# Kernel optimization log

Measured on AMD Instinct MI355X. Metric: run time of the kernel, lower is better.

Reference implementation:

```python
import jax, jax.numpy as jnp
import numpy as np

B, NV, L = 64, 8, 1024
P = 16            # patch_len == stride (non-overlapping)
D, H, DFF = 768, 12, 3072
K = D // H        # head dim 64
T = L // P        # 64 patches per sequence
N = B * NV        # 512 flattened sequences


def _ln(x, g, b, eps=1e-5):
    m = x.mean(-1, keepdims=True)
    v = x.var(-1, keepdims=True)
    return (x - m) / jnp.sqrt(v + eps) * g + b


def _pos_emb():
    pos = jnp.arange(T, dtype=jnp.float32)[:, None]
    div = jnp.exp(jnp.arange(0, D, 2, dtype=jnp.float32) * (-np.log(10000.0) / D))
    pe = jnp.zeros((T, D), jnp.float32)
    pe = pe.at[:, 0::2].set(jnp.sin(pos * div))
    pe = pe.at[:, 1::2].set(jnp.cos(pos * div))
    return pe


def setup_inputs() -> dict:
    key = jax.random.key(0)
    ks = jax.random.split(key, 24)
    rn = lambda k, s: jax.random.normal(k, s, jnp.float32) * 0.02
    return dict(
        x=jax.random.normal(ks[0], (B, NV, L), jnp.float32),
        W_patch=rn(ks[1], (P, D)), b_patch=jnp.zeros((D,), jnp.float32),
        ln1_g=jnp.ones((D,), jnp.float32), ln1_b=jnp.zeros((D,), jnp.float32),
        ln2_g=jnp.ones((D,), jnp.float32), ln2_b=jnp.zeros((D,), jnp.float32),
        mu_r=jax.random.uniform(ks[2], (D,), jnp.float32),
        mu_w=jax.random.uniform(ks[3], (D,), jnp.float32),
        mu_k=jax.random.uniform(ks[4], (D,), jnp.float32),
        mu_v=jax.random.uniform(ks[5], (D,), jnp.float32),
        mu_a=jax.random.uniform(ks[6], (D,), jnp.float32),
        mu_g=jax.random.uniform(ks[7], (D,), jnp.float32),
        mu_c=jax.random.uniform(ks[8], (D,), jnp.float32),
        Wr=rn(ks[9], (D, D)), Wk=rn(ks[10], (D, D)), Wv=rn(ks[11], (D, D)),
        Wg=rn(ks[12], (D, D)), Ww=rn(ks[13], (D, D)), w0=rn(ks[14], (D,)),
        Wa=rn(ks[15], (D, D)), a0=jnp.zeros((D,), jnp.float32),
        Wo=rn(ks[16], (D, D)),
        gn_g=jnp.ones((D,), jnp.float32), gn_b=jnp.zeros((D,), jnp.float32),
        Wc1=rn(ks[17], (D, DFF)), Wc2=rn(ks[18], (DFF, D)),
        W_proj=rn(ks[19], (D, P)), b_proj=jnp.zeros((P,), jnp.float32),
    )


def reference(x, W_patch, b_patch, ln1_g, ln1_b, ln2_g, ln2_b,
              mu_r, mu_w, mu_k, mu_v, mu_a, mu_g, mu_c,
              Wr, Wk, Wv, Wg, Ww, w0, Wa, a0, Wo, gn_g, gn_b,
              Wc1, Wc2, W_proj, b_proj):
    # --- patch embedding (stride == patch_len -> plain reshape) ---
    patches = x.reshape(B, NV, T, P).reshape(N, T, P)
    h = patches @ W_patch + b_patch + _pos_emb()        # [N, T, D]

    # --- RWKV7 time mixing ---
    xx = _ln(h, ln1_g, ln1_b)
    sh = jnp.pad(xx[:, :-1], ((0, 0), (1, 0), (0, 0)))  # token shift
    lerp = lambda mu: xx + (sh - xx) * mu
    r = (lerp(mu_r) @ Wr).reshape(N, T, H, K)
    k = (lerp(mu_k) @ Wk).reshape(N, T, H, K)
    v = (lerp(mu_v) @ Wv).reshape(N, T, H, K)
    w = jnp.exp(-jnp.exp(lerp(mu_w) @ Ww + w0)).reshape(N, T, H, K)  # decay in (0,1)
    a = jax.nn.sigmoid(lerp(mu_a) @ Wa + a0).reshape(N, T, H, K)     # in-context lr
    g = jax.nn.sigmoid(lerp(mu_g) @ Wg)                              # output gate [N,T,D]
    kk = k / (jnp.linalg.norm(k, axis=-1, keepdims=True) + 1e-6)     # removal key

    seq = tuple(jnp.transpose(t, (1, 0, 2, 3)) for t in (r, w, k, v, kk, a))

    def step(S, inp):
        # S: [N, H, V, K] value-by-key state (generalized delta rule)
        r_t, w_t, k_t, v_t, kk_t, a_t = inp
        S = S * w_t[:, :, None, :]
        sa = jnp.einsum('nhvk,nhk->nhv', S, kk_t)
        S = S - jnp.einsum('nhv,nhk->nhvk', sa, kk_t * a_t) \
              + jnp.einsum('nhv,nhk->nhvk', v_t, k_t)
        y = jnp.einsum('nhvk,nhk->nhv', S, r_t)
        return S, y

    S0 = jnp.zeros((N, H, K, K), x.dtype)
    _, ys = jax.lax.scan(step, S0, seq)
    y = jnp.transpose(ys, (1, 0, 2, 3))                 # [N, T, H, K]

    # per-head group norm (RWKV7 uses eps = 64e-5)
    m = y.mean(-1, keepdims=True)
    var = y.var(-1, keepdims=True)
    y = (y - m) / jnp.sqrt(var + 64e-5)
    y = y.reshape(N, T, D) * gn_g + gn_b
    h = h + (y * g) @ Wo

    # --- channel mixing (squared-ReLU FFN) ---
    xc = _ln(h, ln2_g, ln2_b)
    shc = jnp.pad(xc[:, :-1], ((0, 0), (1, 0), (0, 0)))
    xk = xc + (shc - xc) * mu_c
    h = h + jnp.square(jax.nn.relu(xk @ Wc1)) @ Wc2

    # --- projection back to patch space ---
    return h @ W_proj + b_proj                          # [N, T, P]
```

## Files before the change

kernel.cpp:

```cpp
#include <hip/hip_runtime.h>
#include <hip/hip_bf16.h>
#include <math.h>

typedef unsigned short u16;
typedef unsigned int u32;
typedef _Float16 f16x8 __attribute__((ext_vector_type(8)));
typedef float f32x4 __attribute__((ext_vector_type(4)));

#define DEV static __device__ __forceinline__

constexpr int D = 768;
constexpr int HH = 12;
constexpr int KD = 64;
constexpr int T = 64;
constexpr int NSEQ = 512;
constexpr int MROWS = NSEQ * T;
constexpr int DFF = 3072;
constexpr int PP = 16;

DEV u16 f2h(float f){ union{_Float16 h; u16 u;} c; c.h = (_Float16)f; return c.u; }
DEV float h2f(u16 u){ union{u16 u; _Float16 h;} c; c.u = u; return (float)c.h; }
DEV void gld_lds16(const u16* g, u16* l){
  __builtin_amdgcn_global_load_lds((const __attribute__((address_space(1))) void*)g,
                                   (__attribute__((address_space(3))) void*)l, 16, 0, 0);
}
DEV int lsw(int row, int kgrp){ return row * 32 + ((((row >> 2) ^ row) & 3) ^ kgrp) * 8; }

struct TpArgs { const float* src[7]; u16* dst[7]; };
__global__ __launch_bounds__(256) void k_transpose7(TpArgs a){
  __shared__ float tile[32][33];
  int z = blockIdx.z;
  const float* W = a.src[z];
  u16* WT = a.dst[z];
  int c0 = blockIdx.x * 32, r0 = blockIdx.y * 32;
  int tx = threadIdx.x, ty = threadIdx.y;
  #pragma unroll
  for (int i = 0; i < 32; i += 8)
    tile[ty + i][tx] = W[(size_t)(r0 + ty + i) * D + (c0 + tx)];
  __syncthreads();
  #pragma unroll
  for (int i = 0; i < 32; i += 8)
    WT[(size_t)(c0 + ty + i) * D + (r0 + tx)] = f2h(tile[tx][ty + i]);
}

__global__ __launch_bounds__(256) void k_transpose(const float* __restrict__ W, u16* __restrict__ WT,
                                                   int R, int C){
  __shared__ float tile[32][33];
  int c0 = blockIdx.x * 32, r0 = blockIdx.y * 32;
  int tx = threadIdx.x, ty = threadIdx.y;
  #pragma unroll
  for (int i = 0; i < 32; i += 8)
    tile[ty + i][tx] = W[(size_t)(r0 + ty + i) * C + (c0 + tx)];
  __syncthreads();
  #pragma unroll
  for (int i = 0; i < 32; i += 8)
    WT[(size_t)(c0 + ty + i) * R + (r0 + tx)] = f2h(tile[tx][ty + i]);
}

__global__ void k_pe(float* __restrict__ pe){
  int idx = blockIdx.x * 256 + threadIdx.x;
  if (idx >= T * D) return;
  int t = idx / D, d = idx % D;
  float dv = __expf((float)(d & ~1) * (-9.210340371976184f / (float)D));
  float ang = (float)t * dv;
  pe[idx] = (d & 1) ? cosf(ang) : sinf(ang);
}

struct MuArgs { const float* mu[6]; };
__global__ __launch_bounds__(256) void k_mu16(MuArgs a, u16* __restrict__ mu16){
  int z = blockIdx.x;
  #pragma unroll
  for (int j = 0; j < 3; j++){
    int d = threadIdx.x + j * 256;
    mu16[z * D + d] = f2h(a.mu[z][d]);
  }
}

__global__ __launch_bounds__(256) void k_patch_ln(const float* __restrict__ x, const float* __restrict__ Wp,
                                                  const float* __restrict__ bp, const float* __restrict__ pe,
                                                  const float* __restrict__ g, const float* __restrict__ b,
                                                  float* __restrict__ h, u16* __restrict__ xx16){
  int lane = threadIdx.x & 63;
  int row = blockIdx.x * 4 + (threadIdx.x >> 6);
  int t = row & (T - 1);
  const float* xr = x + (size_t)row * PP;
  float xs[PP];
  #pragma unroll
  for (int p = 0; p < PP; p++) xs[p] = xr[p];
  float v[12], s = 0.f, sq = 0.f;
  #pragma unroll
  for (int j = 0; j < 12; j++){
    int d = lane + j * 64;
    float acc = bp[d] + pe[t * D + d];
    #pragma unroll
    for (int p = 0; p < PP; p++) acc = fmaf(xs[p], Wp[p * D + d], acc);
    v[j] = acc; s += acc; sq = fmaf(acc, acc, sq);
  }
  #pragma unroll
  for (int o = 32; o; o >>= 1){ s += __shfl_xor(s, o); sq += __shfl_xor(sq, o); }
  float mean = s * (1.f / 768.f);
  float rstd = rsqrtf(sq * (1.f / 768.f) - mean * mean + 1e-5f);
  float* hrow = h + (size_t)row * D;
  u16* xrow = xx16 + (size_t)row * D;
  #pragma unroll
  for (int j = 0; j < 12; j++){
    int d = lane + j * 64;
    hrow[d] = v[j];
    xrow[d] = f2h((v[j] - mean) * rstd * g[d] + b[d]);
  }
}

__global__ __launch_bounds__(256) void k_ln2(const float* __restrict__ X, const float* __restrict__ g,
                                             const float* __restrict__ b, const float* __restrict__ mu,
                                             u16* __restrict__ out){
  int lane = threadIdx.x & 63;
  int row = blockIdx.x * 4 + (threadIdx.x >> 6);
  int t = row & (T - 1);
  const float* xr = X + (size_t)row * D;
  float v[12], s = 0.f, sq = 0.f;
  #pragma unroll
  for (int j = 0; j < 12; j++){ v[j] = xr[lane + j * 64]; s += v[j]; sq += v[j] * v[j]; }
  #pragma unroll
  for (int o = 32; o; o >>= 1){ s += __shfl_xor(s, o); sq += __shfl_xor(sq, o); }
  float mean = s * (1.f / 768.f);
  float rstd = rsqrtf(sq * (1.f / 768.f) - mean * mean + 1e-5f);
  float p[12], meanp = 0.f, rstdp = 0.f;
  if (t){
    const float* xp = xr - D;
    float sp = 0.f, sqp = 0.f;
    #pragma unroll
    for (int j = 0; j < 12; j++){ p[j] = xp[lane + j * 64]; sp += p[j]; sqp += p[j] * p[j]; }
    #pragma unroll
    for (int o = 32; o; o >>= 1){ sp += __shfl_xor(sp, o); sqp += __shfl_xor(sqp, o); }
    meanp = sp * (1.f / 768.f);
    rstdp = rsqrtf(sqp * (1.f / 768.f) - meanp * meanp + 1e-5f);
  }
  u16* orow = out + (size_t)row * D;
  #pragma unroll
  for (int j = 0; j < 12; j++){
    int d = lane + j * 64;
    float cm = (v[j] - mean) * rstd * g[d] + b[d];
    float cp = t ? (p[j] - meanp) * rstdp * g[d] + b[d] : 0.f;
    orow[d] = f2h(cm + (cp - cm) * mu[d]);
  }
}

template<int ACT>
__global__ __launch_bounds__(256) void k_g16(const u16* __restrict__ A, const u16* __restrict__ BT,
                                             u16* __restrict__ outH, float* __restrict__ outF,
                                             int Kd, int Nc){
  __shared__ __align__(16) u16 As[128 * 32];
  __shared__ __align__(16) u16 Bs[128 * 32];
  int tid = threadIdx.x;
  int m0 = blockIdx.x * 128, n0 = blockIdx.y * 128;
  int wv = tid >> 6, lane = tid & 63;
  int wr = (wv >> 1) * 64, wc = (wv & 1) * 64;
  int lr = lane & 15, kgrp = lane >> 4;
  int r0 = wv * 16 + (lane >> 2);
  int cbg = ((((r0 >> 2) ^ r0) & 3) ^ (lane & 3)) * 8;
  const u16* sA0 = A + (size_t)(m0 + r0) * Kd + cbg;
  const u16* sA1 = A + (size_t)(m0 + r0 + 64) * Kd + cbg;
  const u16* sB0 = BT + (size_t)(n0 + r0) * Kd + cbg;
  const u16* sB1 = BT + (size_t)(n0 + r0 + 64) * Kd + cbg;
  int cb = (lane & 3) * 8;
  u16* dA0 = As + r0 * 32 + cb;
  u16* dA1 = As + (r0 + 64) * 32 + cb;
  u16* dB0 = Bs + r0 * 32 + cb;
  u16* dB1 = Bs + (r0 + 64) * 32 + cb;
  f32x4 acc[4][4] = {};

  for (int k0 = 0; k0 < Kd; k0 += 32){
    __syncthreads();
    gld_lds16(sA0 + k0, dA0);
    gld_lds16(sA1 + k0, dA1);
    gld_lds16(sB0 + k0, dB0);
    gld_lds16(sB1 + k0, dB1);
    __syncthreads();
    f16x8 af[4], bf[4];
    #pragma unroll
    for (int mi = 0; mi < 4; mi++) af[mi] = *(const f16x8*)&As[lsw(wr + mi * 16 + lr, kgrp)];
    #pragma unroll
    for (int ni = 0; ni < 4; ni++) bf[ni] = *(const f16x8*)&Bs[lsw(wc + ni * 16 + lr, kgrp)];
    #pragma unroll
    for (int mi = 0; mi < 4; mi++){
      #pragma unroll
      for (int ni = 0; ni < 4; ni++){
        acc[mi][ni] = __builtin_amdgcn_mfma_f32_16x16x32_f16(af[mi], bf[ni], acc[mi][ni], 0, 0, 0);
      }
    }
  }

  int rowb = m0 + wr + (lane >> 4) * 4;
  int colb = n0 + wc + lr;
  #pragma unroll
  for (int mi = 0; mi < 4; mi++){
    #pragma unroll
    for (int ni = 0; ni < 4; ni++){
      int gcol = colb + ni * 16;
      #pragma unroll
      for (int i = 0; i < 4; i++){
        int grow = rowb + mi * 16 + i;
        float xv = acc[mi][ni][i];
        size_t o = (size_t)grow * Nc + gcol;
        if (ACT == 3){ float rl = fmaxf(xv, 0.f); outH[o] = f2h(rl * rl); }
        else outF[o] += xv;
      }
    }
  }
}

struct MixArgs {
  const u16* b[6]; const float* bias[6]; const u16* mu16;
  u16* outh[6]; int act[6];
};
__global__ __launch_bounds__(256) void k_mix_lerp(const u16* __restrict__ X16, MixArgs args, int Kd, int Nc){
  __shared__ __align__(16) u16 As[128 * 32];
  __shared__ __align__(16) u16 Bs[128 * 32];
  int tid = threadIdx.x, z = blockIdx.z;
  const u16* BT = args.b[z];
  const u16* mu16 = args.mu16 + z * D;
  int m0 = blockIdx.x * 128, n0 = blockIdx.y * 128;
  int wv = tid >> 6, lane = tid & 63;
  int wr = (wv >> 1) * 64, wc = (wv & 1) * 64;
  int lr = lane & 15, kgrp = lane >> 4;
  int r0 = wv * 16 + (lane >> 2);
  int cbg = ((((r0 >> 2) ^ r0) & 3) ^ (lane & 3)) * 8;
  const u16* sB0 = BT + (size_t)(n0 + r0) * Kd + cbg;
  const u16* sB1 = BT + (size_t)(n0 + r0 + 64) * Kd + cbg;
  int cb = (lane & 3) * 8;
  u16* dB0 = Bs + r0 * 32 + cb;
  u16* dB1 = Bs + (r0 + 64) * 32 + cb;
  f32x4 acc[4][4] = {};

  for (int k0 = 0; k0 < Kd; k0 += 32){
    __syncthreads();
    gld_lds16(sB0 + k0, dB0);
    gld_lds16(sB1 + k0, dB1);
    #pragma unroll
    for (int pass = 0; pass < 2; pass++){
      int c = pass * 256 + tid;
      int rr = c >> 2, cgrp = c & 3, c8 = cgrp * 8;
      int row = m0 + rr;
      bool tnz = (row & (T - 1)) != 0;
      const u16* src = X16 + (size_t)row * Kd + k0 + c8;
      f16x8 cur = *(const f16x8*)src;
      f16x8 m8 = *(const f16x8*)(mu16 + k0 + c8);
      f16x8 res;
      if (tnz){
        f16x8 prv = *(const f16x8*)(src - Kd);
        res = cur + (prv - cur) * m8;
      } else {
        res = cur - cur * m8;
      }
      *(f16x8*)&As[lsw(rr, cgrp)] = res;
    }
    __syncthreads();
    f16x8 af[4], bf[4];
    #pragma unroll
    for (int mi = 0; mi < 4; mi++) af[mi] = *(const f16x8*)&As[lsw(wr + mi * 16 + lr, kgrp)];
    #pragma unroll
    for (int ni = 0; ni < 4; ni++) bf[ni] = *(const f16x8*)&Bs[lsw(wc + ni * 16 + lr, kgrp)];
    #pragma unroll
    for (int mi = 0; mi < 4; mi++){
      #pragma unroll
      for (int ni = 0; ni < 4; ni++){
        acc[mi][ni] = __builtin_amdgcn_mfma_f32_16x16x32_f16(af[mi], bf[ni], acc[mi][ni], 0, 0, 0);
      }
    }
  }

  int act = args.act[z];
  const float* bias = args.bias[z];
  u16* outh = args.outh[z];
  int rowb = m0 + wr + (lane >> 4) * 4;
  int colb = n0 + wc + lr;
  #pragma unroll
  for (int mi = 0; mi < 4; mi++){
    #pragma unroll
    for (int ni = 0; ni < 4; ni++){
      int gcol = colb + ni * 16;
      float bv = bias ? bias[gcol] : 0.f;
      #pragma unroll
      for (int i = 0; i < 4; i++){
        int grow = rowb + mi * 16 + i;
        float xv = acc[mi][ni][i] + bv;
        size_t o = (size_t)grow * Nc + gcol;
        if (act == 2) xv = 1.f / (1.f + __expf(-xv));
        outh[o] = f2h(xv);
      }
    }
  }
}

constexpr int TS = 8;
__global__ __launch_bounds__(256) void k_rwkv(const u16* __restrict__ rb16, const u16* __restrict__ wp16,
                                              const u16* __restrict__ kb16, const u16* __restrict__ vb,
                                              const u16* __restrict__ ab, const u16* __restrict__ gbuf,
                                              const float* __restrict__ gng, const float* __restrict__ gnb,
                                              u16* __restrict__ yg){
  __shared__ __align__(16) float ls_w[TS][64], ls_k[TS][64], ls_r[TS][64];
  __shared__ float ls_v[TS][64];
  __shared__ float ls_kk[TS][64], ls_ka[TS][64];
  __shared__ float sa_red[2][4][64];
  __shared__ float y_red[2][4][64];
  int nh = blockIdx.x;
  int n = nh / HH, hh = nh - n * HH;
  int tid = threadIdx.x;
  int wv = __builtin_amdgcn_readfirstlane(tid >> 6);
  int lane = tid & 63;
  float S[16];
  #pragma unroll
  for (int i = 0; i < 16; i++) S[i] = 0.f;
  int dcol = hh * KD + lane;
  float gscale = gng[dcol], gshift = gnb[dcol];
  size_t hbase = (size_t)n * T * D + hh * KD;
  int jbase = wv * 16;
  int strow = tid >> 5;
  int stcol = (tid & 31) * 2;
  for (int tt = 0; tt < T; tt += TS){
    __syncthreads();
    size_t gofs = hbase + (size_t)(tt + strow) * D + stcol;
    u32 w2 = *(const u32*)(wp16 + gofs);
    u32 k2 = *(const u32*)(kb16 + gofs);
    u32 r2 = *(const u32*)(rb16 + gofs);
    u32 v2 = *(const u32*)(vb + gofs);
    u32 a2 = *(const u32*)(ab + gofs);
    float k0 = h2f((u16)(k2 & 0xffffu));
    float k1 = h2f((u16)(k2 >> 16));
    float ss = fmaf(k0, k0, k1 * k1);
    #pragma unroll
    for (int o = 16; o; o >>= 1) ss += __shfl_xor(ss, o);
    float inv = 1.f / (sqrtf(ss) + 1e-6f);
    float kk0 = k0 * inv, kk1 = k1 * inv;
    ls_w[strow][stcol]     = __expf(-__expf(h2f((u16)(w2 & 0xffffu))));
    ls_w[strow][stcol + 1] = __expf(-__expf(h2f((u16)(w2 >> 16))));
    ls_k[strow][stcol]     = k0;
    ls_k[strow][stcol + 1] = k1;
    ls_r[strow][stcol]     = h2f((u16)(r2 & 0xffffu));
    ls_r[strow][stcol + 1] = h2f((u16)(r2 >> 16));
    ls_v[strow][stcol]     = h2f((u16)(v2 & 0xffffu));
    ls_v[strow][stcol + 1] = h2f((u16)(v2 >> 16));
    ls_kk[strow][stcol]     = kk0;
    ls_kk[strow][stcol + 1] = kk1;
    ls_ka[strow][stcol]     = kk0 * h2f((u16)(a2 & 0xffffu));
    ls_ka[strow][stcol + 1] = kk1 * h2f((u16)(a2 >> 16));
    __syncthreads();
    for (int s = 0; s < TS; s++){
      int sg = tt + s;
      int pb = sg & 1;
      f32x4 W4[4], KK4[4];
      #pragma unroll
      for (int q = 0; q < 4; q++){
        W4[q]  = *(const f32x4*)&ls_w[s][jbase + q * 4];
        KK4[q] = *(const f32x4*)&ls_kk[s][jbase + q * 4];
      }
      float sap = 0.f;
      #pragma unroll
      for (int q = 0; q < 4; q++){
        #pragma unroll
        for (int i = 0; i < 4; i++){
          S[q * 4 + i] *= W4[q][i];
          sap += S[q * 4 + i] * KK4[q][i];
        }
      }
      sa_red[pb][wv][lane] = sap;
      __syncthreads();
      if (wv == 0 && sg > 0){
        int pp = pb ^ 1;
        float y = y_red[pp][0][lane] + y_red[pp][1][lane] + y_red[pp][2][lane] + y_red[pp][3][lane];
        float s1 = y, s2 = y * y;
        #pragma unroll
        for (int o = 32; o; o >>= 1){ s1 += __shfl_xor(s1, o); s2 += __shfl_xor(s2, o); }
        float mean = s1 * (1.f / 64.f);
        float var = s2 * (1.f / 64.f) - mean * mean;
        float yn = (y - mean) * rsqrtf(var + 64e-5f);
        size_t pidx = hbase + (size_t)(sg - 1) * D + lane;
        float gv = h2f(gbuf[pidx]);
        yg[pidx] = f2h((yn * gscale + gshift) * gv);
      }
      float sa = sa_red[pb][0][lane] + sa_red[pb][1][lane] + sa_red[pb][2][lane] + sa_red[pb][3][lane];
      float nsa = -sa;
      float vl = ls_v[s][lane];
      f32x4 K4[4], KA4[4], R4[4];
      #pragma unroll
      for (int q = 0; q < 4; q++){
        K4[q]  = *(const f32x4*)&ls_k[s][jbase + q * 4];
        KA4[q] = *(const f32x4*)&ls_ka[s][jbase + q * 4];
        R4[q]  = *(const f32x4*)&ls_r[s][jbase + q * 4];
      }
      float yp = 0.f;
      #pragma unroll
      for (int q = 0; q < 4; q++){
        #pragma unroll
        for (int i = 0; i < 4; i++){
          S[q * 4 + i] = fmaf(vl, K4[q][i], S[q * 4 + i]);
          S[q * 4 + i] = fmaf(nsa, KA4[q][i], S[q * 4 + i]);
          yp += S[q * 4 + i] * R4[q][i];
        }
      }
      y_red[pb][wv][lane] = yp;
    }
  }
  __syncthreads();
  if (wv == 0){
    int pp = (T - 1) & 1;
    float y = y_red[pp][0][lane] + y_red[pp][1][lane] + y_red[pp][2][lane] + y_red[pp][3][lane];
    float s1 = y, s2 = y * y;
    #pragma unroll
    for (int o = 32; o; o >>= 1){ s1 += __shfl_xor(s1, o); s2 += __shfl_xor(s2, o); }
    float mean = s1 * (1.f / 64.f);
    float var = s2 * (1.f / 64.f) - mean * mean;
    float yn = (y - mean) * rsqrtf(var + 64e-5f);
    size_t pidx = hbase + (size_t)(T - 1) * D + lane;
    float gv = h2f(gbuf[pidx]);
    yg[pidx] = f2h((yn * gscale + gshift) * gv);
  }
}

__global__ __launch_bounds__(256) void k_proj(const float* __restrict__ Hb, const float* __restrict__ Wp,
                                              const float* __restrict__ bp, float* __restrict__ out){
  int lane = threadIdx.x & 63;
  int row = blockIdx.x * 4 + (threadIdx.x >> 6);
  int p = lane & 15, q = lane >> 4;
  const float* hr = Hb + (size_t)row * D;
  float acc = 0.f;
  #pragma unroll 8
  for (int i = 0; i < 192; i++){
    int d = q * 192 + i;
    acc = fmaf(hr[d], Wp[d * PP + p], acc);
  }
  acc += __shfl_xor(acc, 16);
  acc += __shfl_xor(acc, 32);
  if (q == 0) out[(size_t)row * PP + p] = acc + bp[p];
}

extern "C" void kernel_launch(void* const* d_in, const int* in_sizes, int n_in,
                              void* d_out, int out_size, void* d_ws, size_t ws_size,
                              hipStream_t stream){
  (void)in_sizes; (void)n_in; (void)out_size;
  const float* x       = (const float*)d_in[0];
  const float* W_patch = (const float*)d_in[1];
  const float* b_patch = (const float*)d_in[2];
  const float* ln1_g   = (const float*)d_in[3];
  const float* ln1_b   = (const float*)d_in[4];
  const float* ln2_g   = (const float*)d_in[5];
  const float* ln2_b   = (const float*)d_in[6];
  const float* mu_r    = (const float*)d_in[7];
  const float* mu_w    = (const float*)d_in[8];
  const float* mu_k    = (const float*)d_in[9];
  const float* mu_v    = (const float*)d_in[10];
  const float* mu_a    = (const float*)d_in[11];
  const float* mu_g    = (const float*)d_in[12];
  const float* mu_c    = (const float*)d_in[13];
  const float* Wr      = (const float*)d_in[14];
  const float* Wk      = (const float*)d_in[15];
  const float* Wv      = (const float*)d_in[16];
  const float* Wg      = (const float*)d_in[17];
  const float* Ww      = (const float*)d_in[18];
  const float* w0      = (const float*)d_in[19];
  const float* Wa      = (const float*)d_in[20];
  const float* a0      = (const float*)d_in[21];
  const float* Wo      = (const float*)d_in[22];
  const float* gn_g    = (const float*)d_in[23];
  const float* gn_b    = (const float*)d_in[24];
  const float* Wc1     = (const float*)d_in[25];
  const float* Wc2     = (const float*)d_in[26];
  const float* W_proj  = (const float*)d_in[27];
  const float* b_proj  = (const float*)d_in[28];
  float* out = (float*)d_out;

  char* ws = (char*)d_ws;
  size_t off = 0;
  auto alloc = [&](size_t bytes) -> char* {
    char* p = ws + off;
    off = (off + bytes + 255) & ~(size_t)255;
    return p;
  };

  const size_t WB = (size_t)D * D * 2;
  u16* WrT  = (u16*)alloc(WB);
  u16* WwT  = (u16*)alloc(WB);
  u16* WkT  = (u16*)alloc(WB);
  u16* WvT  = (u16*)alloc(WB);
  u16* WaT  = (u16*)alloc(WB);
  u16* WgT  = (u16*)alloc(WB);
  u16* WoT  = (u16*)alloc(WB);
  u16* Wc1T = (u16*)alloc((size_t)D * DFF * 2);
  u16* Wc2T = (u16*)alloc((size_t)DFF * D * 2);
  float* pe = (float*)alloc((size_t)T * D * 4);
  u16* mu16 = (u16*)alloc((size_t)6 * D * 2);
  size_t wend = off;

  int nch = 1;
  size_t Mc = MROWS;
  while (nch < 128){
    size_t need = wend + Mc * 13824 + 64 * 256;
    if (need <= ws_size) break;
    nch *= 2;
    Mc >>= 1;
  }
  float* hbuf = (float*)alloc(Mc * 768 * 4);
  u16* xx     = (u16*)alloc(Mc * 768 * 2);
  u16* wp     = (u16*)alloc(Mc * 768 * 2);
  u16* rb     = (u16*)alloc(Mc * 768 * 2);
  u16* kb     = (u16*)alloc(Mc * 768 * 2);
  u16* vb     = (u16*)alloc(Mc * 768 * 2);
  u16* ab     = (u16*)alloc(Mc * 768 * 2);
  u16* gb     = (u16*)alloc(Mc * 768 * 2);
  u16* ygb = ab;
  u16* mid = xx;
  u16* xkb = gb;

  dim3 tb(32, 8);
  TpArgs ta;
  ta.src[0] = Wr; ta.dst[0] = WrT;
  ta.src[1] = Ww; ta.dst[1] = WwT;
  ta.src[2] = Wk; ta.dst[2] = WkT;
  ta.src[3] = Wv; ta.dst[3] = WvT;
  ta.src[4] = Wa; ta.dst[4] = WaT;
  ta.src[5] = Wg; ta.dst[5] = WgT;
  ta.src[6] = Wo; ta.dst[6] = WoT;
  k_transpose7<<<dim3(24, 24, 7), tb, 0, stream>>>(ta);
  k_transpose<<<dim3(96, 24), tb, 0, stream>>>(Wc1, Wc1T, D, DFF);
  k_transpose<<<dim3(24, 96), tb, 0, stream>>>(Wc2, Wc2T, DFF, D);
  k_pe<<<dim3(192), dim3(256), 0, stream>>>(pe);
  MuArgs ma;
  ma.mu[0] = mu_r; ma.mu[1] = mu_w; ma.mu[2] = mu_k;
  ma.mu[3] = mu_v; ma.mu[4] = mu_a; ma.mu[5] = mu_g;
  k_mu16<<<dim3(6), dim3(256), 0, stream>>>(ma, mu16);

  MixArgs margs;
  const u16* wts[6] = {WrT, WwT, WkT, WvT, WaT, WgT};
  const float* bss[6] = {nullptr, w0, nullptr, nullptr, a0, nullptr};
  u16* oh[6] = {rb, wp, kb, vb, ab, gb};
  int acts[6] = {0, 1, 0, 0, 2, 2};
  margs.mu16 = mu16;
  for (int z = 0; z < 6; z++){
    margs.b[z] = wts[z];
    margs.bias[z] = bss[z];
    margs.outh[z] = oh[z];
    margs.act[z] = acts[z];
  }

  for (int c = 0; c < nch; ++c){
    const float* xc = x + (size_t)c * Mc * PP;
    float* outc = out + (size_t)c * Mc * PP;
    int mcb = (int)(Mc / 128);

    k_patch_ln<<<dim3((int)(Mc / 4)), dim3(256), 0, stream>>>(xc, W_patch, b_patch, pe, ln1_g, ln1_b, hbuf, xx);

    k_mix_lerp<<<dim3(mcb, 6, 6), 256, 0, stream>>>(xx, margs, D, D);

    k_rwkv<<<dim3((int)(Mc / T) * HH), dim3(256), 0, stream>>>(rb, wp, kb, vb, ab, gb, gn_g, gn_b, ygb);

    k_g16<4><<<dim3(mcb, 6), 256, 0, stream>>>(ygb, WoT, nullptr, hbuf, D, D);

    k_ln2<<<dim3((int)(Mc / 4)), dim3(256), 0, stream>>>(hbuf, ln2_g, ln2_b, mu_c, xkb);
    k_g16<3><<<dim3(mcb, DFF / 128), 256, 0, stream>>>(xkb, Wc1T, mid, nullptr, D, DFF);
    k_g16<4><<<dim3(mcb, 6), 256, 0, stream>>>(mid, Wc2T, nullptr, hbuf, DFF, D);

    k_proj<<<dim3((int)(Mc / 4)), dim3(256), 0, stream>>>(hbuf, W_proj, b_proj, outc);
  }
}
```

Measured before the change: 1.737 ms.

## Double-buffer LDS tiles in GEMM and mix-lerp kernels to overlap loads with MFMA

Both the plain fp16 GEMM and the token-shift lerp GEMM now keep two LDS buffers for the A and B tiles. The next K-slice is prefetched (via global_load_lds, or register loads followed by the lerp and an LDS store) while MFMAs run on the current slice, and each iteration needs one barrier instead of two. This is meant to hide global-load latency behind compute. In exchange the kernels use twice the LDS, which may lower occupancy, and the lerp kernel holds more registers live across the loop.

```diff
diff --git a/kernel.cpp b/kernel.cpp
--- a/kernel.cpp
+++ b/kernel.cpp
@@ -149,8 +149,8 @@
 __global__ __launch_bounds__(256) void k_g16(const u16* __restrict__ A, const u16* __restrict__ BT,
                                              u16* __restrict__ outH, float* __restrict__ outF,
                                              int Kd, int Nc){
-  __shared__ __align__(16) u16 As[128 * 32];
-  __shared__ __align__(16) u16 Bs[128 * 32];
+  __shared__ __align__(16) u16 As[2][128 * 32];
+  __shared__ __align__(16) u16 Bs[2][128 * 32];
   int tid = threadIdx.x;
   int m0 = blockIdx.x * 128, n0 = blockIdx.y * 128;
   int wv = tid >> 6, lane = tid & 63;
@@ -163,24 +163,29 @@
   const u16* sB0 = BT + (size_t)(n0 + r0) * Kd + cbg;
   const u16* sB1 = BT + (size_t)(n0 + r0 + 64) * Kd + cbg;
   int cb = (lane & 3) * 8;
-  u16* dA0 = As + r0 * 32 + cb;
-  u16* dA1 = As + (r0 + 64) * 32 + cb;
-  u16* dB0 = Bs + r0 * 32 + cb;
-  u16* dB1 = Bs + (r0 + 64) * 32 + cb;
+  int o0 = r0 * 32 + cb, o1 = (r0 + 64) * 32 + cb;
   f32x4 acc[4][4] = {};
-
-  for (int k0 = 0; k0 < Kd; k0 += 32){
-    __syncthreads();
-    gld_lds16(sA0 + k0, dA0);
-    gld_lds16(sA1 + k0, dA1);
-    gld_lds16(sB0 + k0, dB0);
-    gld_lds16(sB1 + k0, dB1);
-    __syncthreads();
+  int NT = Kd >> 5;
+
+  gld_lds16(sA0, &As[0][o0]);
+  gld_lds16(sA1, &As[0][o1]);
+  gld_lds16(sB0, &Bs[0][o0]);
+  gld_lds16(sB1, &Bs[0][o1]);
+  __syncthreads();
+  int cur = 0;
+  for (int kt = 0; kt < NT; kt++){
+    if (kt + 1 < NT){
+      int k0 = (kt + 1) << 5;
+      gld_lds16(sA0 + k0, &As[cur ^ 1][o0]);
+      gld_lds16(sA1 + k0, &As[cur ^ 1][o1]);
+      gld_lds16(sB0 + k0, &Bs[cur ^ 1][o0]);
+      gld_lds16(sB1 + k0, &Bs[cur ^ 1][o1]);
+    }
     f16x8 af[4], bf[4];
     #pragma unroll
-    for (int mi = 0; mi < 4; mi++) af[mi] = *(const f16x8*)&As[lsw(wr + mi * 16 + lr, kgrp)];
-    #pragma unroll
-    for (int ni = 0; ni < 4; ni++) bf[ni] = *(const f16x8*)&Bs[lsw(wc + ni * 16 + lr, kgrp)];
+    for (int mi = 0; mi < 4; mi++) af[mi] = *(const f16x8*)&As[cur][lsw(wr + mi * 16 + lr, kgrp)];
+    #pragma unroll
+    for (int ni = 0; ni < 4; ni++) bf[ni] = *(const f16x8*)&Bs[cur][lsw(wc + ni * 16 + lr, kgrp)];
     #pragma unroll
     for (int mi = 0; mi < 4; mi++){
       #pragma unroll
@@ -188,6 +193,8 @@
         acc[mi][ni] = __builtin_amdgcn_mfma_f32_16x16x32_f16(af[mi], bf[ni], acc[mi][ni], 0, 0, 0);
       }
     }
+    __syncthreads();
+    cur ^= 1;
   }
 
   int rowb = m0 + wr + (lane >> 4) * 4;
@@ -214,8 +221,8 @@
   u16* outh[6]; int act[6];
 };
 __global__ __launch_bounds__(256) void k_mix_lerp(const u16* __restrict__ X16, MixArgs args, int Kd, int Nc){
-  __shared__ __align__(16) u16 As[128 * 32];
-  __shared__ __align__(16) u16 Bs[128 * 32];
+  __shared__ __align__(16) u16 As[2][128 * 32];
+  __shared__ __align__(16) u16 Bs[2][128 * 32];
   int tid = threadIdx.x, z = blockIdx.z;
   const u16* BT = args.b[z];
   const u16* mu16 = args.mu16 + z * D;
@@ -228,38 +235,54 @@
   const u16* sB0 = BT + (size_t)(n0 + r0) * Kd + cbg;
   const u16* sB1 = BT + (size_t)(n0 + r0 + 64) * Kd + cbg;
   int cb = (lane & 3) * 8;
-  u16* dB0 = Bs + r0 * 32 + cb;
-  u16* dB1 = Bs + (r0 + 64) * 32 + cb;
+  int o0 = r0 * 32 + cb, o1 = (r0 + 64) * 32 + cb;
+  int rr0 = tid >> 2, cg0 = tid & 3;
+  int rr1 = (256 + tid) >> 2, cg1 = (256 + tid) & 3;
+  bool tz0 = ((m0 + rr0) & (T - 1)) != 0;
+  bool tz1 = ((m0 + rr1) & (T - 1)) != 0;
+  const u16* srcA0 = X16 + (size_t)(m0 + rr0) * Kd + cg0 * 8;
+  const u16* srcA1 = X16 + (size_t)(m0 + rr1) * Kd + cg1 * 8;
+  int wsl0 = lsw(rr0, cg0), wsl1 = lsw(rr1, cg1);
   f32x4 acc[4][4] = {};
-
-  for (int k0 = 0; k0 < Kd; k0 += 32){
-    __syncthreads();
-    gld_lds16(sB0 + k0, dB0);
-    gld_lds16(sB1 + k0, dB1);
-    #pragma unroll
-    for (int pass = 0; pass < 2; pass++){
-      int c = pass * 256 + tid;
-      int rr = c >> 2, cgrp = c & 3, c8 = cgrp * 8;
-      int row = m0 + rr;
-      bool tnz = (row & (T - 1)) != 0;
-      const u16* src = X16 + (size_t)row * Kd + k0 + c8;
-      f16x8 cur = *(const f16x8*)src;
-      f16x8 m8 = *(const f16x8*)(mu16 + k0 + c8);
-      f16x8 res;
-      if (tnz){
-        f16x8 prv = *(const f16x8*)(src - Kd);
-        res = cur + (prv - cur) * m8;
-      } else {
-        res = cur - cur * m8;
-      }
-      *(f16x8*)&As[lsw(rr, cgrp)] = res;
-    }
-    __syncthreads();
+  int NT = Kd >> 5;
+
+  gld_lds16(sB0, &Bs[0][o0]);
+  gld_lds16(sB1, &Bs[0][o1]);
+  {
+    f16x8 c0 = *(const f16x8*)srcA0;
+    f16x8 m0v = *(const f16x8*)(mu16 + cg0 * 8);
+    f16x8 p0 = {};
+    if (tz0) p0 = *(const f16x8*)(srcA0 - Kd);
+    *(f16x8*)&As[0][wsl0] = c0 + (p0 - c0) * m0v;
+    f16x8 c1 = *(const f16x8*)srcA1;
+    f16x8 m1v = *(const f16x8*)(mu16 + cg1 * 8);
+    f16x8 p1 = {};
+    if (tz1) p1 = *(const f16x8*)(srcA1 - Kd);
+    *(f16x8*)&As[0][wsl1] = c1 + (p1 - c1) * m1v;
+  }
+  __syncthreads();
+  int cur = 0;
+  for (int kt = 0; kt < NT; kt++){
+    bool hn = (kt + 1 < NT);
+    f16x8 nc0, np0, nm0, nc1, np1, nm1;
+    if (hn){
+      int k0 = (kt + 1) << 5;
+      gld_lds16(sB0 + k0, &Bs[cur ^ 1][o0]);
+      gld_lds16(sB1 + k0, &Bs[cur ^ 1][o1]);
+      nc0 = *(const f16x8*)(srcA0 + k0);
+      nm0 = *(const f16x8*)(mu16 + k0 + cg0 * 8);
+      np0 = f16x8{};
+      if (tz0) np0 = *(const f16x8*)(srcA0 + k0 - Kd);
+      nc1 = *(const f16x8*)(srcA1 + k0);
+      nm1 = *(const f16x8*)(mu16 + k0 + cg1 * 8);
+      np1 = f16x8{};
+      if (tz1) np1 = *(const f16x8*)(srcA1 + k0 - Kd);
+    }
     f16x8 af[4], bf[4];
     #pragma unroll
-    for (int mi = 0; mi < 4; mi++) af[mi] = *(const f16x8*)&As[lsw(wr + mi * 16 + lr, kgrp)];
-    #pragma unroll
-    for (int ni = 0; ni < 4; ni++) bf[ni] = *(const f16x8*)&Bs[lsw(wc + ni * 16 + lr, kgrp)];
+    for (int mi = 0; mi < 4; mi++) af[mi] = *(const f16x8*)&As[cur][lsw(wr + mi * 16 + lr, kgrp)];
+    #pragma unroll
+    for (int ni = 0; ni < 4; ni++) bf[ni] = *(const f16x8*)&Bs[cur][lsw(wc + ni * 16 + lr, kgrp)];
     #pragma unroll
     for (int mi = 0; mi < 4; mi++){
       #pragma unroll
@@ -267,6 +290,12 @@
         acc[mi][ni] = __builtin_amdgcn_mfma_f32_16x16x32_f16(af[mi], bf[ni], acc[mi][ni], 0, 0, 0);
       }
     }
+    if (hn){
+      *(f16x8*)&As[cur ^ 1][wsl0] = nc0 + (np0 - nc0) * nm0;
+      *(f16x8*)&As[cur ^ 1][wsl1] = nc1 + (np1 - nc1) * nm1;
+    }
+    __syncthreads();
+    cur ^= 1;
   }
 
   int act = args.act[z];
```

Result: faster. 1.608 ms (median of 2 runs) (-7.4%).
